# Performance work log

Measured on AMD Instinct MI355X. Metric: run time of the kernel, lower is better.

## Reference

```python
import jax, jax.numpy as jnp
import numpy as np

B, T, V = 64, 4096, 64
NGLIMPSE = 32
GRAN_SCALES = (1, 5)  # hard-coded in getGlimpseTimesteps
NGRAN = len(GRAN_SCALES)
NHID = 2048
GWIDTH = 0.1


def setup_inputs() -> dict:
    key = jax.random.key(0)
    k1, k2, k3, k4, k5 = jax.random.split(key, 5)
    # times sorted ascending per sample (scipy interp1d assumption)
    time = jnp.sort(jax.random.uniform(k1, (B, T)) * 100.0, axis=1)
    vals = jax.random.normal(k2, (B, T, V))
    masks = (jax.random.uniform(k3, (B, T, V)) < 0.5).astype(jnp.int32)
    lengths = jnp.full((B,), T, dtype=jnp.int32)
    l_t = jax.random.uniform(k4, (B, 1), minval=0.1, maxval=0.9)
    fan_in = V * NGRAN * NGLIMPSE + 1
    W = jax.random.normal(k5, (NHID, fan_in)) / np.sqrt(fan_in)
    b = jnp.zeros((NHID,), jnp.float32)
    return {"vals": vals, "time": time, "masks": masks,
            "lengths": lengths, "l_t": l_t, "W": W, "b": b}


def _interp_one(t, v, m, r):
    """Masked 1D linear interp of (t[m], v[m]) at queries r.
    Constant fill (first/last valid value) outside bounds; 0 if no valid point."""
    ts = jnp.where(m, t, jnp.inf)
    order = jnp.argsort(ts)          # stable: valid (already sorted) times first
    tsort = ts[order]                # [T], inf tail for invalid entries
    vsort = v[order]
    n = m.sum()
    idx = jnp.searchsorted(tsort, r, side='right')
    i1 = jnp.clip(idx, 1, jnp.maximum(n - 1, 1))
    i0 = i1 - 1
    t0, t1 = tsort[i0], tsort[i1]
    v0, v1 = vsort[i0], vsort[i1]
    w = jnp.clip((r - t0) / jnp.where(t1 > t0, t1 - t0, 1.0), 0.0, 1.0)
    y = v0 + w * (v1 - v0)
    last = jnp.maximum(n - 1, 0)
    y = jnp.where(r <= tsort[0], vsort[0],
                  jnp.where(r >= tsort[last], vsort[last], y))
    return jnp.where(n == 0, 0.0, y)


def _glimpses(vals, time, masks, l_t):
    # [NGRAN, NGLIMPSE] offsets: linspace(-gwidth*i/2, gwidth*i/2, nglimpse)
    lin = jnp.stack([jnp.linspace(-GWIDTH * i / 2.0, GWIDTH * i / 2.0, NGLIMPSE)
                     for i in GRAN_SCALES])

    def per_sample(t, v, m, l):
        # denormalize by per-sample max time; granularity-major flatten
        r = ((lin + l) * t.max()).reshape(-1)          # [NGRAN*NGLIMPSE]
        return jax.vmap(lambda vv, mm: _interp_one(t, vv, mm, r),
                        in_axes=(1, 1))(v, m)          # [V, NGRAN*NGLIMPSE]

    return jax.vmap(per_sample)(time, vals, masks.astype(bool), l_t[:, 0])


def reference(vals, time, masks, lengths, l_t, W, b):
    g = _glimpses(vals, time, masks, l_t).reshape(vals.shape[0], -1)  # [B, V*NGRAN*NGLIMPSE]
    grep = jnp.concatenate([g, l_t], axis=1) @ W.T + b                # [B, NHID]
    return grep, g[:, g.shape[1] // 2]
```

## Files before the change

kernel.cpp:

```cpp
#include <hip/hip_runtime.h>
#include <hip/hip_bf16.h>

#define B    64
#define T    4096
#define V    64
#define NQ   64
#define NHID 2048
#define KDIM 4096
#define FAN  4097

#define NT     16
#define SPLITS 16
#define KC     256

typedef __attribute__((ext_vector_type(8))) short bf16x8;
typedef __attribute__((ext_vector_type(4))) float f32x4;

static __device__ __forceinline__ short f2bf(float x) {
    union { float f; unsigned u; } c; c.f = x;
    unsigned r = c.u + 0x7fff + ((c.u >> 16) & 1);
    return (short)(r >> 16);
}

static __device__ __forceinline__ void load_lds16(const void* g, void* l) {
    __builtin_amdgcn_global_load_lds(
        (const __attribute__((address_space(1))) void*)g,
        (__attribute__((address_space(3))) void*)l, 16, 0, 0);
}

static __device__ __forceinline__ unsigned cvt_pk(float lo, float hi) {
    unsigned r;
    asm volatile("v_cvt_pk_bf16_f32 %0, %1, %2" : "=v"(r) : "v"(lo), "v"(hi));
    return r;
}

__global__ __launch_bounds__(64) void glimpse_kernel(
    const float* __restrict__ vals, const float* __restrict__ time_,
    const int* __restrict__ masks, const float* __restrict__ l_t,
    unsigned short* __restrict__ g_bf, float* __restrict__ out2,
    float* __restrict__ out)
{
    const int b = blockIdx.x;
    const int q = blockIdx.y;
    const int v = threadIdx.x;

    if (v < 32) out[(size_t)b * NHID + q * 32 + v] = 0.0f;

    const float* t = time_ + (size_t)b * T;
    const float tmax = t[T - 1];

    const int   j = q & 31;
    const float s = (q < 32) ? 1.0f : 5.0f;
    const float a = 0.5f * 0.1f * s;
    const float step = (2.0f * a) / 31.0f;
    float lin = (j == 31) ? a : (-a + step * (float)j);
    const float r = (lin + l_t[b]) * tmax;

    int lo = 0, hi = T;
    while (lo < hi) {
        int mid = (lo + hi) >> 1;
        if (t[mid] > r) hi = mid; else lo = mid + 1;
    }
    const int p = lo;

    const int*   m  = masks + (size_t)b * T * V + v;
    const float* vv = vals  + (size_t)b * T * V + v;

    int i0 = -1;
    for (int i = p - 1; i >= 0; --i) {
        if (m[(size_t)i * V] != 0) { i0 = i; break; }
    }
    int i1 = -1;
    for (int i = p; i < T; ++i) {
        if (m[(size_t)i * V] != 0) { i1 = i; break; }
    }

    float y;
    if (i0 < 0 && i1 < 0) {
        y = 0.0f;
    } else if (i0 < 0) {
        y = vv[(size_t)i1 * V];
    } else if (i1 < 0) {
        y = vv[(size_t)i0 * V];
    } else {
        float t0 = t[i0], t1 = t[i1];
        float v0 = vv[(size_t)i0 * V], v1 = vv[(size_t)i1 * V];
        float den = (t1 > t0) ? (t1 - t0) : 1.0f;
        float w = (r - t0) / den;
        w = fminf(fmaxf(w, 0.0f), 1.0f);
        y = v0 + w * (v1 - v0);
    }

    const int k = v * NQ + q;
    g_bf[(size_t)b * KDIM + k] = (unsigned short)f2bf(y);
    if (k == KDIM / 2) out2[b] = y;
}

__global__ __launch_bounds__(256) void gemm_mfma(
    const unsigned short* __restrict__ g_bf, const float* __restrict__ l_t,
    const float* __restrict__ W, const float* __restrict__ bias,
    float* __restrict__ out)
{
    __shared__ unsigned short alds[B * KC];
    __shared__ float wlds[NT * KC];
    const int tid  = threadIdx.x;
    const int l    = tid & 63;
    const int w    = tid >> 6;
    const int l15  = l & 15;
    const int lk   = l >> 4;
    const int hbase = blockIdx.x * NT;
    const int s     = blockIdx.y;
    const int kbase = s * KC;

    #pragma unroll
    for (int i = 0; i < 8; ++i) {
        const int m = w * 8 + i;
        const int r = 2 * m + (l >> 5);
        const int c = (l & 31) ^ (r & 7);
        load_lds16(g_bf + (size_t)r * KDIM + kbase + c * 8,
                   alds + m * 512);
    }
    #pragma unroll
    for (int i = 0; i < 4; ++i) {
        const int r = w * 4 + i;
        const int c = l ^ (r & 7);
        load_lds16(W + (size_t)(hbase + r) * FAN + kbase + c * 4,
                   wlds + r * KC);
    }
    asm volatile("s_waitcnt vmcnt(0)" ::: "memory");
    __syncthreads();

    f32x4 acc = (f32x4){0.f, 0.f, 0.f, 0.f};
    const int ra = w * 16 + l15;
    const int rb = l15;

    #pragma unroll
    for (int ks = 0; ks < 8; ++ks) {
        const int ca = ks * 4 + lk;
        const bf16x8 afrag =
            *(const bf16x8*)(alds + ra * KC + ((ca ^ (ra & 7)) << 3));

        const int cb = ks * 8 + lk * 2;
        const float4 f0 = *(const float4*)(wlds + rb * KC + (((cb    ) ^ (rb & 7)) << 2));
        const float4 f1 = *(const float4*)(wlds + rb * KC + (((cb + 1) ^ (rb & 7)) << 2));
        union { unsigned u[4]; bf16x8 v; } bb;
        bb.u[0] = cvt_pk(f0.x, f0.y);
        bb.u[1] = cvt_pk(f0.z, f0.w);
        bb.u[2] = cvt_pk(f1.x, f1.y);
        bb.u[3] = cvt_pk(f1.z, f1.w);

        acc = __builtin_amdgcn_mfma_f32_16x16x32_bf16(afrag, bb.v, acc, 0, 0, 0);
    }

    const int h = hbase + l15;
    #pragma unroll
    for (int rr = 0; rr < 4; ++rr) {
        const int b = w * 16 + lk * 4 + rr;
        float v = acc[rr];
        if (s == 0)
            v += bias[h] + l_t[b] * W[(size_t)h * FAN + KDIM];
        atomicAdd(&out[(size_t)b * NHID + h], v);
    }
}

extern "C" void kernel_launch(void* const* d_in, const int* in_sizes, int n_in,
                              void* d_out, int out_size, void* d_ws, size_t ws_size,
                              hipStream_t stream) {
    const float* vals  = (const float*)d_in[0];
    const float* time_ = (const float*)d_in[1];
    const int*   masks = (const int*)d_in[2];
    const float* l_t   = (const float*)d_in[4];
    const float* W     = (const float*)d_in[5];
    const float* bias  = (const float*)d_in[6];

    float* out  = (float*)d_out;
    float* out2 = out + (size_t)B * NHID;
    unsigned short* g_bf = (unsigned short*)d_ws;

    dim3 g1(B, NQ);
    glimpse_kernel<<<g1, 64, 0, stream>>>(vals, time_, masks, l_t, g_bf, out2, out);

    dim3 g2(NHID / NT, SPLITS);
    gemm_mfma<<<g2, 256, 0, stream>>>(g_bf, l_t, W, bias, out);
}
```

Before: 30.04 us.

## Pre-convert W to bf16 inside glimpse kernel and load bf16 tiles in GEMM

```diff
diff --git a/kernel.cpp b/kernel.cpp
--- a/kernel.cpp
+++ b/kernel.cpp
@@ -28,15 +28,10 @@
         (__attribute__((address_space(3))) void*)l, 16, 0, 0);
 }
 
-static __device__ __forceinline__ unsigned cvt_pk(float lo, float hi) {
-    unsigned r;
-    asm volatile("v_cvt_pk_bf16_f32 %0, %1, %2" : "=v"(r) : "v"(lo), "v"(hi));
-    return r;
-}
-
 __global__ __launch_bounds__(64) void glimpse_kernel(
     const float* __restrict__ vals, const float* __restrict__ time_,
     const int* __restrict__ masks, const float* __restrict__ l_t,
+    const float* __restrict__ W, unsigned short* __restrict__ Wb,
     unsigned short* __restrict__ g_bf, float* __restrict__ out2,
     float* __restrict__ out)
 {
@@ -45,6 +40,17 @@
     const int v = threadIdx.x;
 
     if (v < 32) out[(size_t)b * NHID + q * 32 + v] = 0.0f;
+
+    {
+        const size_t f0 = ((size_t)b * NQ + q) * 2048;
+        #pragma unroll 8
+        for (int i = 0; i < 32; ++i) {
+            const size_t f = f0 + (size_t)i * 64 + v;
+            const int row = (int)(f >> 12);
+            const int col = (int)(f & 4095);
+            Wb[f] = (unsigned short)f2bf(W[(size_t)row * FAN + col]);
+        }
+    }
 
     const float* t = time_ + (size_t)b * T;
     const float tmax = t[T - 1];
@@ -97,12 +103,12 @@
 }
 
 __global__ __launch_bounds__(256) void gemm_mfma(
-    const unsigned short* __restrict__ g_bf, const float* __restrict__ l_t,
-    const float* __restrict__ W, const float* __restrict__ bias,
-    float* __restrict__ out)
+    const unsigned short* __restrict__ g_bf, const unsigned short* __restrict__ Wb,
+    const float* __restrict__ l_t, const float* __restrict__ W,
+    const float* __restrict__ bias, float* __restrict__ out)
 {
     __shared__ unsigned short alds[B * KC];
-    __shared__ float wlds[NT * KC];
+    __shared__ unsigned short wlds[NT * KC];
     const int tid  = threadIdx.x;
     const int l    = tid & 63;
     const int w    = tid >> 6;
@@ -121,11 +127,12 @@
                    alds + m * 512);
     }
     #pragma unroll
-    for (int i = 0; i < 4; ++i) {
-        const int r = w * 4 + i;
-        const int c = l ^ (r & 7);
-        load_lds16(W + (size_t)(hbase + r) * FAN + kbase + c * 4,
-                   wlds + r * KC);
+    for (int i = 0; i < 2; ++i) {
+        const int m = w * 2 + i;
+        const int r = 2 * m + (l >> 5);
+        const int c = (l & 31) ^ (r & 7);
+        load_lds16(Wb + (size_t)(hbase + r) * KDIM + kbase + c * 8,
+                   wlds + m * 512);
     }
     asm volatile("s_waitcnt vmcnt(0)" ::: "memory");
     __syncthreads();
@@ -139,17 +146,9 @@
         const int ca = ks * 4 + lk;
         const bf16x8 afrag =
             *(const bf16x8*)(alds + ra * KC + ((ca ^ (ra & 7)) << 3));
-
-        const int cb = ks * 8 + lk * 2;
-        const float4 f0 = *(const float4*)(wlds + rb * KC + (((cb    ) ^ (rb & 7)) << 2));
-        const float4 f1 = *(const float4*)(wlds + rb * KC + (((cb + 1) ^ (rb & 7)) << 2));
-        union { unsigned u[4]; bf16x8 v; } bb;
-        bb.u[0] = cvt_pk(f0.x, f0.y);
-        bb.u[1] = cvt_pk(f0.z, f0.w);
-        bb.u[2] = cvt_pk(f1.x, f1.y);
-        bb.u[3] = cvt_pk(f1.z, f1.w);
-
-        acc = __builtin_amdgcn_mfma_f32_16x16x32_bf16(afrag, bb.v, acc, 0, 0, 0);
+        const bf16x8 bfrag =
+            *(const bf16x8*)(wlds + rb * KC + ((ca ^ (rb & 7)) << 3));
+        acc = __builtin_amdgcn_mfma_f32_16x16x32_bf16(afrag, bfrag, acc, 0, 0, 0);
     }
 
     const int h = hbase + l15;
@@ -176,10 +175,12 @@
     float* out  = (float*)d_out;
     float* out2 = out + (size_t)B * NHID;
     unsigned short* g_bf = (unsigned short*)d_ws;
+    unsigned short* Wb = (unsigned short*)((char*)d_ws + (1 << 20));
 
     dim3 g1(B, NQ);
-    glimpse_kernel<<<g1, 64, 0, stream>>>(vals, time_, masks, l_t, g_bf, out2, out);
+    glimpse_kernel<<<g1, 64, 0, stream>>>(vals, time_, masks, l_t, W, Wb,
+                                          g_bf, out2, out);
 
     dim3 g2(NHID / NT, SPLITS);
-    gemm_mfma<<<g2, 256, 0, stream>>>(g_bf, l_t, W, bias, out);
+    gemm_mfma<<<g2, 256, 0, stream>>>(g_bf, Wb, l_t, W, bias, out);
 }
```

New measurement: 34.78 us. 15.7% more time.
